# Optimization experiments

Hardware: AMD Instinct MI355X
Metric: run time of the kernel (lower is better)

## Reference

```python
import jax, jax.numpy as jnp
import numpy as np

B, S, H = 1, 4096, 2048
NH, NKV, HD = 16, 4, 128  # query heads, kv heads, head_dim
THETA = 1000000.0
NEG = -1e9


def setup_inputs() -> dict:
    key = jax.random.key(0)
    ks = jax.random.split(key, 5)
    hidden_states = jax.random.normal(ks[0], (B, S, H), jnp.float32) * 0.02
    Wq = jax.random.normal(ks[1], (H, NH * HD), jnp.float32) * 0.02
    Wk = jax.random.normal(ks[2], (H, NKV * HD), jnp.float32) * 0.02
    Wv = jax.random.normal(ks[3], (H, NKV * HD), jnp.float32) * 0.02
    Wo = jax.random.normal(ks[4], (H, H), jnp.float32) * 0.02
    # additive causal mask [B,1,S,S]
    causal = jnp.tril(jnp.ones((S, S), bool))
    attention_mask = jnp.where(causal, 0.0, NEG).astype(jnp.float32)[None, None]
    position_ids = jnp.arange(S, dtype=jnp.int32)[None]
    return dict(hidden_states=hidden_states, Wq=Wq, Wk=Wk, Wv=Wv, Wo=Wo,
                attention_mask=attention_mask, position_ids=position_ids)


def _rotate_half(x):
    return jnp.concatenate([-x[..., HD // 2:], x[..., :HD // 2]], axis=-1)


def reference(hidden_states, Wq, Wk, Wv, Wo, attention_mask, position_ids):
    # projections -> [B, heads, S, HD]
    q = (hidden_states @ Wq).reshape(B, S, NH, HD).transpose(0, 2, 1, 3)
    k = (hidden_states @ Wk).reshape(B, S, NKV, HD).transpose(0, 2, 1, 3)
    v = (hidden_states @ Wv).reshape(B, S, NKV, HD).transpose(0, 2, 1, 3)

    # RoPE (HF style: freqs duplicated across halves, rotate_half)
    inv_freq = 1.0 / (THETA ** (jnp.arange(0, HD, 2, dtype=jnp.float32) / HD))
    freqs = position_ids.astype(jnp.float32)[..., None] * inv_freq  # [B,S,HD/2]
    emb = jnp.concatenate([freqs, freqs], axis=-1)                  # [B,S,HD]
    cos = jnp.cos(emb)[:, None].astype(q.dtype)                     # [B,1,S,HD]
    sin = jnp.sin(emb)[:, None].astype(q.dtype)
    q = q * cos + _rotate_half(q) * sin
    k = k * cos + _rotate_half(k) * sin

    # GQA: repeat each kv head consecutively (matches torch repeat_kv)
    rep = NH // NKV
    k = jnp.repeat(k, rep, axis=1)
    v = jnp.repeat(v, rep, axis=1)

    scale = 1.0 / jnp.sqrt(jnp.float32(HD))
    scores = jnp.einsum('bhqd,bhkd->bhqk', q, k) * scale + attention_mask
    attn = jax.nn.softmax(scores.astype(jnp.float32), axis=-1).astype(q.dtype)
    out = jnp.einsum('bhqk,bhkd->bhqd', attn, v)  # [B,NH,S,HD]
    out = out.transpose(0, 2, 1, 3).reshape(B, S, H)
    return out @ Wo
```

## Files before the change

### kernel.cpp

```cpp
#include <hip/hip_runtime.h>
#include <stdint.h>

typedef uint16_t u16;
typedef __bf16  bf16x8 __attribute__((ext_vector_type(8)));
typedef float   f32x4  __attribute__((ext_vector_type(4)));
typedef uint16_t u16x8 __attribute__((ext_vector_type(8), may_alias));

typedef const __attribute__((address_space(1))) void* gas_p;
typedef __attribute__((address_space(3))) void* las_p;

__device__ __forceinline__ void load_lds16(const void* g, void* l) {
    __builtin_amdgcn_global_load_lds((gas_p)g, (las_p)l, 16, 0, 0);
}

__device__ __forceinline__ u16 f2bf(float f) {
    uint32_t u = __builtin_bit_cast(uint32_t, f);
    u += 0x7FFFu + ((u >> 16) & 1u);
    return (u16)(u >> 16);
}
__device__ __forceinline__ float bf2f(u16 h) {
    uint32_t u = ((uint32_t)h) << 16;
    return __builtin_bit_cast(float, u);
}
__device__ __forceinline__ bf16x8 ld_frag(const u16* p) {
    u16x8 t = *(const u16x8*)p;
    return __builtin_bit_cast(bf16x8, t);
}

__global__ __launch_bounds__(256) void convert_hidden(const float* __restrict__ in,
                                                      u16* __restrict__ out, int n8) {
    int i = blockIdx.x * 256 + threadIdx.x;
    if (i >= n8) return;
    const float* p = in + (size_t)i * 8;
    u16x8 o;
#pragma unroll
    for (int j = 0; j < 8; j++) o[j] = f2bf(p[j]);
    *(u16x8*)(out + (size_t)i * 8) = o;
}

__global__ __launch_bounds__(256) void transpose_cvt(const float* __restrict__ in,
                                                     u16* __restrict__ out,
                                                     int R, int C) {
    __shared__ u16 tile[64][65];
    const int tx = threadIdx.x;
    const int bc = blockIdx.x * 64;
    const int br = blockIdx.y * 64;
#pragma unroll
    for (int i = 0; i < 16; i++) {
        int idx = tx + i * 256;
        int r = idx >> 6, c = idx & 63;
        tile[r][c] = f2bf(in[(size_t)(br + r) * C + bc + c]);
    }
    __syncthreads();
#pragma unroll
    for (int i = 0; i < 16; i++) {
        int idx = tx + i * 256;
        int r = idx >> 6, c = idx & 63;
        out[(size_t)(bc + r) * R + br + c] = tile[c][r];
    }
}

__global__ __launch_bounds__(256) void transpose_b16(const u16* __restrict__ in,
                                                     u16* __restrict__ out,
                                                     int R, int C, int ldin, int off) {
    __shared__ u16 tile[64][65];
    const int tx = threadIdx.x;
    const int bc = blockIdx.x * 64;
    const int br = blockIdx.y * 64;
#pragma unroll
    for (int i = 0; i < 16; i++) {
        int idx = tx + i * 256;
        int r = idx >> 6, c = idx & 63;
        tile[r][c] = in[(size_t)(br + r) * ldin + off + bc + c];
    }
    __syncthreads();
#pragma unroll
    for (int i = 0; i < 16; i++) {
        int idx = tx + i * 256;
        int r = idx >> 6, c = idx & 63;
        out[(size_t)(bc + r) * R + br + c] = tile[c][r];
    }
}

#define TM 128
#define TN 128
#define TK 32

__global__ __launch_bounds__(256) void gemm_qkv(const u16* __restrict__ A,
                                                const u16* __restrict__ WqT,
                                                const u16* __restrict__ WkvT,
                                                u16* __restrict__ Qb,
                                                u16* __restrict__ KVb) {
    __shared__ u16 As[TM * TK];
    __shared__ u16 Bs[TN * TK];
    const int K = 2048;
    const int tid  = threadIdx.x;
    const int wave = tid >> 6;
    const int lane = tid & 63;
    const int l15  = lane & 15;
    const int quad = lane >> 4;
    const int m0 = blockIdx.y * TM;
    const int n0 = blockIdx.x * TN;
    const u16* Bt;
    u16* C;
    int ldC, cbase;
    if (n0 < 2048) { Bt = WqT + (size_t)n0 * K;          C = Qb;  ldC = 2048; cbase = n0; }
    else           { Bt = WkvT + (size_t)(n0 - 2048) * K; C = KVb; ldC = 1024; cbase = n0 - 2048; }
    const int wm = (wave >> 1) * 64;
    const int wn = (wave & 1) * 64;

    f32x4 acc[4][4] = {};

    const int srow = tid >> 2;
    const int scol = (tid & 3) * 8;
    const u16* Ap0 = A  + (size_t)(m0 + srow) * K + scol;
    const u16* Ap1 = A  + (size_t)(m0 + 64 + srow) * K + scol;
    const u16* Bp0 = Bt + (size_t)srow * K + scol;
    const u16* Bp1 = Bt + (size_t)(64 + srow) * K + scol;
    u16* AsD0 = As + wave * 512;
    u16* AsD1 = As + 2048 + wave * 512;
    u16* BsD0 = Bs + wave * 512;
    u16* BsD1 = Bs + 2048 + wave * 512;

    for (int k0 = 0; k0 < K; k0 += TK) {
        load_lds16(Ap0 + k0, AsD0);
        load_lds16(Ap1 + k0, AsD1);
        load_lds16(Bp0 + k0, BsD0);
        load_lds16(Bp1 + k0, BsD1);
        __syncthreads();
        bf16x8 af[4], bfr[4];
#pragma unroll
        for (int i = 0; i < 4; i++)
            af[i] = ld_frag(&As[(wm + i * 16 + l15) * TK + quad * 8]);
#pragma unroll
        for (int j = 0; j < 4; j++)
            bfr[j] = ld_frag(&Bs[(wn + j * 16 + l15) * TK + quad * 8]);
#pragma unroll
        for (int i = 0; i < 4; i++)
#pragma unroll
            for (int j = 0; j < 4; j++)
                acc[i][j] = __builtin_amdgcn_mfma_f32_16x16x32_bf16(af[i], bfr[j], acc[i][j], 0, 0, 0);
        __syncthreads();
    }
#pragma unroll
    for (int i = 0; i < 4; i++)
#pragma unroll
        for (int j = 0; j < 4; j++)
#pragma unroll
            for (int r = 0; r < 4; r++) {
                int row = m0 + wm + i * 16 + quad * 4 + r;
                int col = cbase + wn + j * 16 + l15;
                C[(size_t)row * ldC + col] = f2bf(acc[i][j][r]);
            }
}

template <bool F32OUT>
__global__ __launch_bounds__(256) void gemm_bt(const u16* __restrict__ A,
                                               const u16* __restrict__ Bt,
                                               void* __restrict__ Cp,
                                               int M, int N, int K) {
    __shared__ u16 As[TM * TK];
    __shared__ u16 Bs[TN * TK];
    const int tid  = threadIdx.x;
    const int wave = tid >> 6;
    const int lane = tid & 63;
    const int l15  = lane & 15;
    const int quad = lane >> 4;
    const int m0 = blockIdx.y * TM;
    const int n0 = blockIdx.x * TN;
    const int wm = (wave >> 1) * 64;
    const int wn = (wave & 1) * 64;

    f32x4 acc[4][4] = {};

    const int srow = tid >> 2;
    const int scol = (tid & 3) * 8;
    const u16* Ap0 = A  + (size_t)(m0 + srow) * K + scol;
    const u16* Ap1 = A  + (size_t)(m0 + 64 + srow) * K + scol;
    const u16* Bp0 = Bt + (size_t)(n0 + srow) * K + scol;
    const u16* Bp1 = Bt + (size_t)(n0 + 64 + srow) * K + scol;
    u16* AsD0 = As + wave * 512;
    u16* AsD1 = As + 2048 + wave * 512;
    u16* BsD0 = Bs + wave * 512;
    u16* BsD1 = Bs + 2048 + wave * 512;

    for (int k0 = 0; k0 < K; k0 += TK) {
        load_lds16(Ap0 + k0, AsD0);
        load_lds16(Ap1 + k0, AsD1);
        load_lds16(Bp0 + k0, BsD0);
        load_lds16(Bp1 + k0, BsD1);
        __syncthreads();
        bf16x8 af[4], bfr[4];
#pragma unroll
        for (int i = 0; i < 4; i++)
            af[i] = ld_frag(&As[(wm + i * 16 + l15) * TK + quad * 8]);
#pragma unroll
        for (int j = 0; j < 4; j++)
            bfr[j] = ld_frag(&Bs[(wn + j * 16 + l15) * TK + quad * 8]);
#pragma unroll
        for (int i = 0; i < 4; i++)
#pragma unroll
            for (int j = 0; j < 4; j++)
                acc[i][j] = __builtin_amdgcn_mfma_f32_16x16x32_bf16(af[i], bfr[j], acc[i][j], 0, 0, 0);
        __syncthreads();
    }
#pragma unroll
    for (int i = 0; i < 4; i++)
#pragma unroll
        for (int j = 0; j < 4; j++)
#pragma unroll
            for (int r = 0; r < 4; r++) {
                int row = m0 + wm + i * 16 + quad * 4 + r;
                int col = n0 + wn + j * 16 + l15;
                if (F32OUT)
                    ((float*)Cp)[(size_t)row * N + col] = acc[i][j][r];
                else
                    ((u16*)Cp)[(size_t)row * N + col] = f2bf(acc[i][j][r]);
            }
}

__global__ __launch_bounds__(256) void rope_kernel(u16* __restrict__ Q,
                                                   u16* __restrict__ KV) {
    int g = blockIdx.x * 256 + threadIdx.x;
    int d = g & 63;
    int row = g >> 6;
    int s = row / 20;
    int hh = row - s * 20;
    u16* buf = (hh < 16) ? (Q + (size_t)s * 2048 + hh * 128)
                         : (KV + (size_t)s * 1024 + (hh - 16) * 128);
    float p = (float)s;
    float angle = p * exp2f((float)d * (-19.931568569324174f / 64.0f));
    float c = cosf(angle), sn = sinf(angle);
    float x0 = bf2f(buf[d]), x1 = bf2f(buf[d + 64]);
    buf[d]      = f2bf(x0 * c - x1 * sn);
    buf[d + 64] = f2bf(x1 * c + x0 * sn);
}

#define SCALE2 0.1275430214486847f
#define PSTR 40

__global__ __launch_bounds__(256, 2) void flash_attn3(const u16* __restrict__ Q,
                                                      const u16* __restrict__ KVb,
                                                      const u16* __restrict__ VT,
                                                      u16* __restrict__ O) {
    __shared__ u16 Ks[8192];
    __shared__ u16 Vs[8192];
    __shared__ u16 Plds[4][2 * 16 * PSTR];
    const int tid  = threadIdx.x;
    const int wave = tid >> 6;
    const int lane = tid & 63;
    const int l15  = lane & 15;
    const int quad = lane >> 4;
    const int bx   = blockIdx.x;
    const int h    = blockIdx.y;
    const int kvh  = h >> 2;
    const int q_lo = bx * 64;
    const int q_hi = (63 - bx) * 64;

    bf16x8 qlo[4], qhi[4];
    {
        const u16* plo = Q + (size_t)(q_lo + wave * 16 + l15) * 2048 + h * 128 + quad * 8;
        const u16* phi = Q + (size_t)(q_hi + wave * 16 + l15) * 2048 + h * 128 + quad * 8;
#pragma unroll
        for (int s4 = 0; s4 < 4; s4++) { qlo[s4] = ld_frag(plo + s4 * 32); qhi[s4] = ld_frag(phi + s4 * 32); }
    }

    f32x4 acc_lo[8] = {}, acc_hi[8] = {};
    float l_lo[4] = {}, l_hi[4] = {};
    const int qt_lo = q_lo + wave * 16;
    const int qt_hi = q_hi + wave * 16;
    const int qrow_lo = qt_lo + quad * 4;
    const int qrow_hi = qt_hi + quad * 4;

    const u16* srcK[4];
    const u16* srcV[4];
#pragma unroll
    for (int r = 0; r < 4; r++) {
        int p = r * 256 + tid;
        int kv = p >> 4;
        srcK[r] = KVb + (size_t)kv * 1024 + kvh * 128 + ((((p & 15) - kv) & 15) * 8);
        int d = p >> 3;
        srcV[r] = VT + (size_t)(kvh * 128 + d) * 4096 + ((((p & 7) - (d & 7)) & 7) * 8);
    }
    u16* PW = &Plds[wave][0];

    const int nkv = 64 - bx;
    const int nlo = bx + 1;

    for (int kvb = 0; kvb < nkv; kvb++) {
        const int kv0 = kvb * 64;
        __syncthreads();
#pragma unroll
        for (int r = 0; r < 4; r++) {
            load_lds16(srcK[r] + (size_t)kv0 * 1024, Ks + r * 2048 + wave * 512);
            load_lds16(srcV[r] + kv0, Vs + r * 2048 + wave * 512);
        }
        __syncthreads();

        const bool do_lo = (kvb < nlo);
        f32x4 svl[4] = {}, svh[4] = {};
#pragma unroll
        for (int s4 = 0; s4 < 4; s4++)
#pragma unroll
            for (int t = 0; t < 4; t++) {
                int row = t * 16 + l15;
                bf16x8 kf = ld_frag(&Ks[row * 128 + (((s4 * 4 + quad) + row) & 15) * 8]);
                svh[t] = __builtin_amdgcn_mfma_f32_16x16x32_bf16(qhi[s4], kf, svh[t], 0, 0, 0);
                if (do_lo)
                    svl[t] = __builtin_amdgcn_mfma_f32_16x16x32_bf16(qlo[s4], kf, svl[t], 0, 0, 0);
            }

#pragma unroll
        for (int tile = 0; tile < 2; tile++) {
            if (tile == 0 && !do_lo) continue;
            const f32x4* sv = (tile == 0) ? svl : svh;
            float* l_i      = (tile == 0) ? l_lo : l_hi;
            f32x4* acc      = (tile == 0) ? acc_lo : acc_hi;
            const int qrow0 = (tile == 0) ? qrow_lo : qrow_hi;

            float pv[4][4];
#pragma unroll
            for (int r = 0; r < 4; r++) {
                int qrow = qrow0 + r;
                float rs = 0.f;
#pragma unroll
                for (int t = 0; t < 4; t++) {
                    float p = exp2f(sv[t][r] * SCALE2);
                    if (kv0 + t * 16 + l15 > qrow) p = 0.f;
                    pv[t][r] = p;
                    rs += p;
                }
#pragma unroll
                for (int off = 1; off < 16; off <<= 1)
                    rs += __shfl_xor(rs, off, 64);
                l_i[r] += rs;
            }
#pragma unroll
            for (int t = 0; t < 2; t++)
#pragma unroll
                for (int r = 0; r < 4; r++)
                    PW[(quad * 4 + r) * PSTR + t * 16 + l15] = f2bf(pv[t][r]);
#pragma unroll
            for (int t = 0; t < 2; t++)
#pragma unroll
                for (int r = 0; r < 4; r++)
                    PW[16 * PSTR + (quad * 4 + r) * PSTR + t * 16 + l15] = f2bf(pv[2 + t][r]);
            bf16x8 pf0 = ld_frag(&PW[l15 * PSTR + quad * 8]);
            bf16x8 pf1 = ld_frag(&PW[16 * PSTR + l15 * PSTR + quad * 8]);
#pragma unroll
            for (int nt = 0; nt < 8; nt++) {
                int row = nt * 16 + l15;
                bf16x8 vf0 = ld_frag(&Vs[row * 64 + ((quad + (row & 7)) & 7) * 8]);
                bf16x8 vf1 = ld_frag(&Vs[row * 64 + (((4 + quad) + (row & 7)) & 7) * 8]);
                acc[nt] = __builtin_amdgcn_mfma_f32_16x16x32_bf16(pf0, vf0, acc[nt], 0, 0, 0);
                acc[nt] = __builtin_amdgcn_mfma_f32_16x16x32_bf16(pf1, vf1, acc[nt], 0, 0, 0);
            }
        }
    }

#pragma unroll
    for (int r = 0; r < 4; r++) {
        float invl = 1.0f / l_lo[r];
        float invh = 1.0f / l_hi[r];
        int rowl = qrow_lo + r, rowh = qrow_hi + r;
#pragma unroll
        for (int nt = 0; nt < 8; nt++) {
            O[(size_t)rowl * 2048 + h * 128 + nt * 16 + l15] = f2bf(acc_lo[nt][r] * invl);
            O[(size_t)rowh * 2048 + h * 128 + nt * 16 + l15] = f2bf(acc_hi[nt][r] * invh);
        }
    }
}

extern "C" void kernel_launch(void* const* d_in, const int* in_sizes, int n_in,
                              void* d_out, int out_size, void* d_ws, size_t ws_size,
                              hipStream_t stream) {
    const float* hidden = (const float*)d_in[0];
    const float* Wq = (const float*)d_in[1];
    const float* Wk = (const float*)d_in[2];
    const float* Wv = (const float*)d_in[3];
    const float* Wo = (const float*)d_in[4];
    float* out = (float*)d_out;

    u16* ws   = (u16*)d_ws;
    u16* Hb   = ws;
    u16* Qb   = Hb   + 8388608;
    u16* KVb  = Qb   + 8388608;
    u16* WqT  = KVb  + 4194304;
    u16* WkvT = WqT  + 4194304;
    u16* VT   = WkvT + 2097152;

    convert_hidden<<<4096, 256, 0, stream>>>(hidden, Hb, 1048576);

    transpose_cvt<<<dim3(32, 32), 256, 0, stream>>>(Wq, WqT, 2048, 2048);
    transpose_cvt<<<dim3(8, 32), 256, 0, stream>>>(Wk, WkvT, 2048, 512);
    transpose_cvt<<<dim3(8, 32), 256, 0, stream>>>(Wv, WkvT + 1048576, 2048, 512);

    gemm_qkv<<<dim3(24, 32), 256, 0, stream>>>(Hb, WqT, WkvT, Qb, KVb);

    u16* WoT = WqT;
    transpose_cvt<<<dim3(32, 32), 256, 0, stream>>>(Wo, WoT, 2048, 2048);

    rope_kernel<<<dim3(20480), 256, 0, stream>>>(Qb, KVb);

    transpose_b16<<<dim3(8, 64), 256, 0, stream>>>(KVb, VT, 4096, 512, 1024, 512);

    u16* Ob = Hb;
    flash_attn3<<<dim3(32, 16), 256, 0, stream>>>(Qb, KVb, VT, Ob);

    gemm_bt<true><<<dim3(16, 32), 256, 0, stream>>>(Ob, WoT, out, 4096, 2048, 2048);
}
```

Before: 464.1 us.

## Rewrite flash attention with 32x32 MFMA, register P transpose, double-buffered KV

Replaces the attention kernel with one where each wave packs its low and high query tiles into a single 32-row 32x32x16 MFMA, computing S^T so the probabilities can be turned into the PV operand in registers via cvt_pk_bf16 and permlane32_swap. This removes the per-wave LDS round trip for P. K/V tiles are double-buffered in LDS so the next block's global-to-LDS loads overlap compute, cutting one barrier per iteration. Masking is specialised per block type (full, diagonal, low-tile-dead), and row sums are reduced at the end via LDS. The cost is wasted MFMA work on dead low-tile rows after the causal boundary, plus doubled LDS use that may affect occupancy.

```diff
diff --git a/kernel.cpp b/kernel.cpp
--- a/kernel.cpp
+++ b/kernel.cpp
@@ -4,7 +4,9 @@
 typedef uint16_t u16;
 typedef __bf16  bf16x8 __attribute__((ext_vector_type(8)));
 typedef float   f32x4  __attribute__((ext_vector_type(4)));
+typedef float   f32x16 __attribute__((ext_vector_type(16)));
 typedef uint16_t u16x8 __attribute__((ext_vector_type(8), may_alias));
+typedef uint32_t u32x4 __attribute__((ext_vector_type(4)));
 
 typedef const __attribute__((address_space(1))) void* gas_p;
 typedef __attribute__((address_space(3))) void* las_p;
@@ -25,6 +27,14 @@
 __device__ __forceinline__ bf16x8 ld_frag(const u16* p) {
     u16x8 t = *(const u16x8*)p;
     return __builtin_bit_cast(bf16x8, t);
+}
+__device__ __forceinline__ uint32_t cvt_pk_bf16(float lo, float hi) {
+    uint32_t r;
+    asm("v_cvt_pk_bf16_f32 %0, %1, %2" : "=v"(r) : "v"(lo), "v"(hi));
+    return r;
+}
+__device__ __forceinline__ void plane32_swap(uint32_t& a, uint32_t& b) {
+    asm("v_permlane32_swap_b32 %0, %1" : "+v"(a), "+v"(b));
 }
 
 __global__ __launch_bounds__(256) void convert_hidden(const float* __restrict__ in,
@@ -237,40 +247,36 @@
 }
 
 #define SCALE2 0.1275430214486847f
-#define PSTR 40
-
-__global__ __launch_bounds__(256, 2) void flash_attn3(const u16* __restrict__ Q,
+
+__global__ __launch_bounds__(256, 2) void flash_attn4(const u16* __restrict__ Q,
                                                       const u16* __restrict__ KVb,
                                                       const u16* __restrict__ VT,
                                                       u16* __restrict__ O) {
-    __shared__ u16 Ks[8192];
-    __shared__ u16 Vs[8192];
-    __shared__ u16 Plds[4][2 * 16 * PSTR];
+    __shared__ u16 Ks[2][8192];
+    __shared__ u16 Vs[2][8192];
+    __shared__ float Llds[4][32];
     const int tid  = threadIdx.x;
     const int wave = tid >> 6;
     const int lane = tid & 63;
-    const int l15  = lane & 15;
-    const int quad = lane >> 4;
+    const int l31  = lane & 31;
+    const int hi8  = lane >> 5;
     const int bx   = blockIdx.x;
     const int h    = blockIdx.y;
     const int kvh  = h >> 2;
     const int q_lo = bx * 64;
     const int q_hi = (63 - bx) * 64;
-
-    bf16x8 qlo[4], qhi[4];
+    const int nlo  = bx + 1;
+    const int nkv  = 64 - bx;
+
+    const int qrow = (l31 < 16) ? (q_lo + wave * 16 + l31)
+                                : (q_hi + wave * 16 + (l31 - 16));
+
+    bf16x8 qf[8];
     {
-        const u16* plo = Q + (size_t)(q_lo + wave * 16 + l15) * 2048 + h * 128 + quad * 8;
-        const u16* phi = Q + (size_t)(q_hi + wave * 16 + l15) * 2048 + h * 128 + quad * 8;
-#pragma unroll
-        for (int s4 = 0; s4 < 4; s4++) { qlo[s4] = ld_frag(plo + s4 * 32); qhi[s4] = ld_frag(phi + s4 * 32); }
-    }
-
-    f32x4 acc_lo[8] = {}, acc_hi[8] = {};
-    float l_lo[4] = {}, l_hi[4] = {};
-    const int qt_lo = q_lo + wave * 16;
-    const int qt_hi = q_hi + wave * 16;
-    const int qrow_lo = qt_lo + quad * 4;
-    const int qrow_hi = qt_hi + quad * 4;
+        const u16* qp = Q + (size_t)qrow * 2048 + h * 128 + hi8 * 8;
+#pragma unroll
+        for (int dk = 0; dk < 8; dk++) qf[dk] = ld_frag(qp + dk * 16);
+    }
 
     const u16* srcK[4];
     const u16* srcV[4];
@@ -282,92 +288,116 @@
         int d = p >> 3;
         srcV[r] = VT + (size_t)(kvh * 128 + d) * 4096 + ((((p & 7) - (d & 7)) & 7) * 8);
     }
-    u16* PW = &Plds[wave][0];
-
-    const int nkv = 64 - bx;
-    const int nlo = bx + 1;
+
+    f32x16 acc[4] = {};
+    float l_run = 0.f;
+
+#pragma unroll
+    for (int r = 0; r < 4; r++) {
+        load_lds16(srcK[r], &Ks[0][r * 2048 + wave * 512]);
+        load_lds16(srcV[r], &Vs[0][r * 2048 + wave * 512]);
+    }
+    asm volatile("s_waitcnt vmcnt(0)" ::: "memory");
+    __syncthreads();
 
     for (int kvb = 0; kvb < nkv; kvb++) {
+        const int cur = kvb & 1;
+        if (kvb + 1 < nkv) {
+            const int kvn = (kvb + 1) * 64;
+#pragma unroll
+            for (int r = 0; r < 4; r++) {
+                load_lds16(srcK[r] + (size_t)kvn * 1024, &Ks[cur ^ 1][r * 2048 + wave * 512]);
+                load_lds16(srcV[r] + kvn, &Vs[cur ^ 1][r * 2048 + wave * 512]);
+            }
+        }
+        const u16* Kb = Ks[cur];
+        const u16* Vb = Vs[cur];
         const int kv0 = kvb * 64;
+        const int mmode = (kvb == nlo - 1 || kvb == nkv - 1) ? 1 : ((kvb >= nlo) ? 2 : 0);
+        const bool lodead = (l31 < 16);
+
+#pragma unroll
+        for (int cc = 0; cc < 2; cc++) {
+            f32x16 sv = {};
+            const int krow = cc * 32 + l31;
+#pragma unroll
+            for (int dk = 0; dk < 8; dk++) {
+                int slot = ((dk * 2 + hi8) + krow) & 15;
+                bf16x8 kf = ld_frag(&Kb[krow * 128 + slot * 8]);
+                sv = __builtin_amdgcn_mfma_f32_32x32x16_bf16(kf, qf[dk], sv, 0, 0, 0);
+            }
+            float p[16];
+            float rs = 0.f;
+            if (mmode == 0) {
+#pragma unroll
+                for (int r = 0; r < 16; r++) {
+                    float pe = exp2f(sv[r] * SCALE2);
+                    p[r] = pe; rs += pe;
+                }
+            } else if (mmode == 1) {
+                const int kvbase = kv0 + cc * 32 + 4 * hi8;
+#pragma unroll
+                for (int r = 0; r < 16; r++) {
+                    float pe = exp2f(sv[r] * SCALE2);
+                    int kvv = kvbase + (r & 3) + 8 * (r >> 2);
+                    if (kvv > qrow) pe = 0.f;
+                    p[r] = pe; rs += pe;
+                }
+            } else {
+#pragma unroll
+                for (int r = 0; r < 16; r++) {
+                    float pe = exp2f(sv[r] * SCALE2);
+                    if (lodead) pe = 0.f;
+                    p[r] = pe; rs += pe;
+                }
+            }
+            l_run += rs;
+
+            uint32_t w0a = cvt_pk_bf16(p[0], p[1]);
+            uint32_t w1a = cvt_pk_bf16(p[2], p[3]);
+            uint32_t w2a = cvt_pk_bf16(p[4], p[5]);
+            uint32_t w3a = cvt_pk_bf16(p[6], p[7]);
+            plane32_swap(w0a, w2a);
+            plane32_swap(w1a, w3a);
+            uint32_t w0b = cvt_pk_bf16(p[8],  p[9]);
+            uint32_t w1b = cvt_pk_bf16(p[10], p[11]);
+            uint32_t w2b = cvt_pk_bf16(p[12], p[13]);
+            uint32_t w3b = cvt_pk_bf16(p[14], p[15]);
+            plane32_swap(w0b, w2b);
+            plane32_swap(w1b, w3b);
+            u32x4 paw0 = {w0a, w1a, w2a, w3a};
+            u32x4 paw1 = {w0b, w1b, w2b, w3b};
+            bf16x8 pa0 = __builtin_bit_cast(bf16x8, paw0);
+            bf16x8 pa1 = __builtin_bit_cast(bf16x8, paw1);
+
+#pragma unroll
+            for (int ks2 = 0; ks2 < 2; ks2++) {
+                bf16x8 pa = ks2 ? pa1 : pa0;
+#pragma unroll
+                for (int nt = 0; nt < 4; nt++) {
+                    int d = nt * 32 + l31;
+                    int slot = ((cc * 4 + ks2 * 2 + hi8) + d) & 7;
+                    bf16x8 vf = ld_frag(&Vb[d * 64 + slot * 8]);
+                    acc[nt] = __builtin_amdgcn_mfma_f32_32x32x16_bf16(pa, vf, acc[nt], 0, 0, 0);
+                }
+            }
+        }
+        asm volatile("s_waitcnt vmcnt(0)" ::: "memory");
         __syncthreads();
-#pragma unroll
-        for (int r = 0; r < 4; r++) {
-            load_lds16(srcK[r] + (size_t)kv0 * 1024, Ks + r * 2048 + wave * 512);
-            load_lds16(srcV[r] + kv0, Vs + r * 2048 + wave * 512);
-        }
-        __syncthreads();
-
-        const bool do_lo = (kvb < nlo);
-        f32x4 svl[4] = {}, svh[4] = {};
-#pragma unroll
-        for (int s4 = 0; s4 < 4; s4++)
-#pragma unroll
-            for (int t = 0; t < 4; t++) {
-                int row = t * 16 + l15;
-                bf16x8 kf = ld_frag(&Ks[row * 128 + (((s4 * 4 + quad) + row) & 15) * 8]);
-                svh[t] = __builtin_amdgcn_mfma_f32_16x16x32_bf16(qhi[s4], kf, svh[t], 0, 0, 0);
-                if (do_lo)
-                    svl[t] = __builtin_amdgcn_mfma_f32_16x16x32_bf16(qlo[s4], kf, svl[t], 0, 0, 0);
-            }
-
-#pragma unroll
-        for (int tile = 0; tile < 2; tile++) {
-            if (tile == 0 && !do_lo) continue;
-            const f32x4* sv = (tile == 0) ? svl : svh;
-            float* l_i      = (tile == 0) ? l_lo : l_hi;
-            f32x4* acc      = (tile == 0) ? acc_lo : acc_hi;
-            const int qrow0 = (tile == 0) ? qrow_lo : qrow_hi;
-
-            float pv[4][4];
-#pragma unroll
-            for (int r = 0; r < 4; r++) {
-                int qrow = qrow0 + r;
-                float rs = 0.f;
-#pragma unroll
-                for (int t = 0; t < 4; t++) {
-                    float p = exp2f(sv[t][r] * SCALE2);
-                    if (kv0 + t * 16 + l15 > qrow) p = 0.f;
-                    pv[t][r] = p;
-                    rs += p;
-                }
-#pragma unroll
-                for (int off = 1; off < 16; off <<= 1)
-                    rs += __shfl_xor(rs, off, 64);
-                l_i[r] += rs;
-            }
-#pragma unroll
-            for (int t = 0; t < 2; t++)
-#pragma unroll
-                for (int r = 0; r < 4; r++)
-                    PW[(quad * 4 + r) * PSTR + t * 16 + l15] = f2bf(pv[t][r]);
-#pragma unroll
-            for (int t = 0; t < 2; t++)
-#pragma unroll
-                for (int r = 0; r < 4; r++)
-                    PW[16 * PSTR + (quad * 4 + r) * PSTR + t * 16 + l15] = f2bf(pv[2 + t][r]);
-            bf16x8 pf0 = ld_frag(&PW[l15 * PSTR + quad * 8]);
-            bf16x8 pf1 = ld_frag(&PW[16 * PSTR + l15 * PSTR + quad * 8]);
-#pragma unroll
-            for (int nt = 0; nt < 8; nt++) {
-                int row = nt * 16 + l15;
-                bf16x8 vf0 = ld_frag(&Vs[row * 64 + ((quad + (row & 7)) & 7) * 8]);
-                bf16x8 vf1 = ld_frag(&Vs[row * 64 + (((4 + quad) + (row & 7)) & 7) * 8]);
-                acc[nt] = __builtin_amdgcn_mfma_f32_16x16x32_bf16(pf0, vf0, acc[nt], 0, 0, 0);
-                acc[nt] = __builtin_amdgcn_mfma_f32_16x16x32_bf16(pf1, vf1, acc[nt], 0, 0, 0);
-            }
-        }
-    }
-
-#pragma unroll
-    for (int r = 0; r < 4; r++) {
-        float invl = 1.0f / l_lo[r];
-        float invh = 1.0f / l_hi[r];
-        int rowl = qrow_lo + r, rowh = qrow_hi + r;
-#pragma unroll
-        for (int nt = 0; nt < 8; nt++) {
-            O[(size_t)rowl * 2048 + h * 128 + nt * 16 + l15] = f2bf(acc_lo[nt][r] * invl);
-            O[(size_t)rowh * 2048 + h * 128 + nt * 16 + l15] = f2bf(acc_hi[nt][r] * invh);
-        }
+    }
+
+    float l_tot = l_run + __shfl_xor(l_run, 32);
+    if (lane < 32) Llds[wave][l31] = l_tot;
+    __syncthreads();
+#pragma unroll
+    for (int r = 0; r < 16; r++) {
+        int cr = (r & 3) + 8 * (r >> 2) + 4 * hi8;
+        float linv = 1.0f / Llds[wave][cr];
+        int row = (cr < 16) ? (q_lo + wave * 16 + cr) : (q_hi + wave * 16 + (cr - 16));
+        u16* op = O + (size_t)row * 2048 + h * 128 + l31;
+#pragma unroll
+        for (int nt = 0; nt < 4; nt++)
+            op[nt * 32] = f2bf(acc[nt][r] * linv);
     }
 }
 
@@ -405,7 +435,7 @@
     transpose_b16<<<dim3(8, 64), 256, 0, stream>>>(KVb, VT, 4096, 512, 1024, 512);
 
     u16* Ob = Hb;
-    flash_attn3<<<dim3(32, 16), 256, 0, stream>>>(Qb, KVb, VT, Ob);
+    flash_attn4<<<dim3(32, 16), 256, 0, stream>>>(Qb, KVb, VT, Ob);
 
     gemm_bt<true><<<dim3(16, 32), 256, 0, stream>>>(Ob, WoT, out, 4096, 2048, 2048);
 }
```

Measured after the change: 461.2 us. About the same (-0.6%).
